# Performance work log

Measured on AMD Instinct MI355X. Metric: run time of the kernel, lower is better.

The kernel has to match this reference:

```python
import jax, jax.numpy as jnp
import numpy as np

H = 4096       # hidden_size
D_IN = 8192    # intermediate_size
N = 16         # ssm_state_size
K = 4          # conv_kernel
R = 256        # time_step_rank
EPS = 1e-6     # mixer_rms_eps


def rms_forward(x, eps=EPS):
    xf = x.astype(jnp.float32)
    var = jnp.mean(xf * xf, axis=-1, keepdims=True)
    return (xf * jax.lax.rsqrt(var + eps)).astype(x.dtype)


def setup_inputs() -> dict:
    key = jax.random.key(0)
    ks = jax.random.split(key, 10)
    s = 0.02
    hidden_states = jax.random.normal(ks[0], (2, 1024, H), dtype=jnp.float32)
    W_in = jax.random.normal(ks[1], (2 * D_IN, H), dtype=jnp.float32) * s
    conv_w = jax.random.normal(ks[2], (D_IN, K), dtype=jnp.float32) * 0.2
    conv_b = jax.random.normal(ks[3], (D_IN,), dtype=jnp.float32) * 0.02
    W_x = jax.random.normal(ks[4], (R + 2 * N, D_IN), dtype=jnp.float32) * s
    W_dt = jax.random.normal(ks[5], (D_IN, R), dtype=jnp.float32) * s
    b_dt = jax.random.normal(ks[6], (D_IN,), dtype=jnp.float32) * 0.02
    A_log = jnp.log(jnp.broadcast_to(jnp.arange(1, N + 1, dtype=jnp.float32)[None, :], (D_IN, N)))
    D = jnp.ones((D_IN,), dtype=jnp.float32)
    W_out = jax.random.normal(ks[7], (H, D_IN), dtype=jnp.float32) * s
    return {"hidden_states": hidden_states, "W_in": W_in, "conv_w": conv_w,
            "conv_b": conv_b, "W_x": W_x, "W_dt": W_dt, "b_dt": b_dt,
            "A_log": A_log, "D": D, "W_out": W_out}


def reference(hidden_states, W_in, conv_w, conv_b, W_x, W_dt, b_dt, A_log, D, W_out):
    b, L, _ = hidden_states.shape
    # in_proj -> split into x and gate  [b, L, d_in] each
    proj = hidden_states @ W_in.T
    x, gate = proj[..., :D_IN], proj[..., D_IN:]
    # depthwise causal conv1d over time (padding K-1, keep first L) + SiLU
    xpad = jnp.pad(x, ((0, 0), (K - 1, 0), (0, 0)))
    xc = conv_b
    for j in range(K):
        xc = xc + conv_w[:, j] * xpad[:, j:j + L, :]
    x = jax.nn.silu(xc)                               # [b, L, d_in]
    # x_proj -> dt / B / C, each RMS-normalized (weightless, FalconMamba)
    ssm = x @ W_x.T                                   # [b, L, R+2N]
    ts, Bm, Cm = ssm[..., :R], ssm[..., R:R + N], ssm[..., R + N:]
    ts = rms_forward(ts)
    Bm = rms_forward(Bm)
    Cm = rms_forward(Cm)
    dt = jax.nn.softplus(ts @ W_dt.T + b_dt)          # [b, L, d_in]
    A = -jnp.exp(A_log.astype(jnp.float32))           # [d_in, N]
    # selective scan over time: state [b, d_in, N]
    def step(state, inp):
        dt_t, B_t, C_t, u_t = inp                     # [b,d],[b,N],[b,N],[b,d]
        dA = jnp.exp(dt_t[..., None] * A)             # [b, d_in, N]
        state = state * dA + (dt_t * u_t)[..., None] * B_t[:, None, :]
        y = jnp.einsum('bdn,bn->bd', state, C_t)
        return state, y
    init = jnp.zeros((b, D_IN, N), dtype=jnp.float32)
    xs = (dt.transpose(1, 0, 2), Bm.transpose(1, 0, 2),
          Cm.transpose(1, 0, 2), x.transpose(1, 0, 2))
    _, ys = jax.lax.scan(step, init, xs)              # [L, b, d_in]
    y = ys.transpose(1, 0, 2) + x * D                 # skip with D
    y = y * jax.nn.silu(gate)                         # gated output
    return y @ W_out.T                                # [b, L, H]
```

## Files before the change

### kernel.cpp

```cpp
#include <hip/hip_runtime.h>
#include <hip/hip_bf16.h>

#define DIN 8192
#define HH 4096
#define BLT 2048
#define LSEQ 1024
#define CL 64
#define NCG 32

typedef unsigned short u16;
typedef __bf16 bf16x8 __attribute__((ext_vector_type(8)));
typedef float f32x4v __attribute__((ext_vector_type(4)));

__device__ __forceinline__ u16 f2b(float f) {
  unsigned u = __float_as_uint(f);
  u += 0x7fff + ((u >> 16) & 1);
  return (u16)(u >> 16);
}
__device__ __forceinline__ float b2f(u16 h) {
  return __uint_as_float(((unsigned)h) << 16);
}

__device__ __forceinline__ void gl_lds16(const u16* g, u16* l) {
  __builtin_amdgcn_global_load_lds(
      (const __attribute__((address_space(1))) void*)g,
      (__attribute__((address_space(3))) void*)l, 16, 0, 0);
}

__device__ __forceinline__ int bsw(int r) { return (r & 3) ^ ((r >> 2) & 3); }

__global__ void cvt_kernel(const float* __restrict__ in, u16* __restrict__ out, long n) {
  long i = ((long)blockIdx.x * blockDim.x + threadIdx.x) * 4;
  long stride = (long)gridDim.x * blockDim.x * 4;
  for (; i < n; i += stride) {
    f32x4v v = *(const f32x4v*)(in + i);
    ushort4 o;
    o.x = f2b(v[0]); o.y = f2b(v[1]); o.z = f2b(v[2]); o.w = f2b(v[3]);
    *(ushort4*)(out + i) = o;
  }
}

__global__ void cvt_pad_kernel(const float* __restrict__ in, u16* __restrict__ out,
                               int rows_in, int cols, long n_out) {
  long i = ((long)blockIdx.x * blockDim.x + threadIdx.x) * 4;
  long stride = (long)gridDim.x * blockDim.x * 4;
  for (; i < n_out; i += stride) {
    long r = i / cols;
    long c = i - r * cols;
    ushort4 o;
    if (r < rows_in) {
      f32x4v v = *(const f32x4v*)(in + r * cols + c);
      o.x = f2b(v[0]); o.y = f2b(v[1]); o.z = f2b(v[2]); o.w = f2b(v[3]);
    } else {
      o.x = 0; o.y = 0; o.z = 0; o.w = 0;
    }
    *(ushort4*)(out + i) = o;
  }
}

__global__ void add2_kernel(const float* __restrict__ a, const float* __restrict__ b,
                            float* __restrict__ o, long n) {
  long i = ((long)blockIdx.x * blockDim.x + threadIdx.x) * 4;
  long stride = (long)gridDim.x * blockDim.x * 4;
  for (; i < n; i += stride) {
    f32x4v va = *(const f32x4v*)(a + i);
    f32x4v vb = *(const f32x4v*)(b + i);
    *(f32x4v*)(o + i) = va + vb;
  }
}

template<int MODE>
__global__ __launch_bounds__(256) void gemm_bt(
    const u16* __restrict__ A, const u16* __restrict__ B, void* __restrict__ Cp,
    int M, int N, int Klen, int lda, const float* __restrict__ bias = nullptr)
{
  __shared__ __align__(16) u16 As[128 * 32];
  __shared__ __align__(16) u16 Bs[128 * 32];
  const int tid = threadIdx.x;
  const int wave = tid >> 6;
  const int lane = tid & 63;
  const int wr = wave >> 1;
  const int wc = wave & 1;
  const long m0 = (long)blockIdx.y * 128;
  const long n0 = (long)blockIdx.x * 128;
  const long kbase = (long)blockIdx.z * Klen;
  const int fr = lane & 15;
  const int fq = lane >> 4;
  const int fs = fq ^ bsw(fr);

  f32x4v acc[4][4];
#pragma unroll
  for (int i = 0; i < 4; ++i)
#pragma unroll
    for (int j = 0; j < 4; ++j) acc[i][j] = (f32x4v){0.f, 0.f, 0.f, 0.f};

  const int srow = tid >> 2;
  const int sseg0 = (tid & 3) ^ bsw(srow);

  for (int k0 = 0; k0 < Klen; k0 += 32) {
#pragma unroll
    for (int i = 0; i < 2; ++i) {
      const int row = srow + i * 64;
      gl_lds16(A + (m0 + row) * (long)lda + kbase + k0 + sseg0 * 8, As + (i * 256 + wave * 64) * 8);
      gl_lds16(B + (n0 + row) * (long)lda + kbase + k0 + sseg0 * 8, Bs + (i * 256 + wave * 64) * 8);
    }
    __syncthreads();
    bf16x8 af[4], bfr[4];
#pragma unroll
    for (int mi = 0; mi < 4; ++mi)
      af[mi] = *(const bf16x8*)(As + (wr * 64 + mi * 16 + fr) * 32 + fs * 8);
#pragma unroll
    for (int ni = 0; ni < 4; ++ni)
      bfr[ni] = *(const bf16x8*)(Bs + (wc * 64 + ni * 16 + fr) * 32 + fs * 8);
#pragma unroll
    for (int mi = 0; mi < 4; ++mi)
#pragma unroll
      for (int ni = 0; ni < 4; ++ni)
        acc[mi][ni] = __builtin_amdgcn_mfma_f32_16x16x32_bf16(af[mi], bfr[ni], acc[mi][ni], 0, 0, 0);
    __syncthreads();
  }

  float* Cf = (float*)Cp + (size_t)blockIdx.z * M * N;
#pragma unroll
  for (int mi = 0; mi < 4; ++mi) {
#pragma unroll
    for (int ni = 0; ni < 4; ++ni) {
      const long col = n0 + wc * 64 + ni * 16 + fr;
#pragma unroll
      for (int r = 0; r < 4; ++r) {
        const long rowi = m0 + wr * 64 + mi * 16 + fq * 4 + r;
        if constexpr (MODE == 0) {
          Cf[rowi * N + col] = acc[mi][ni][r];
        } else {
          const float z = acc[mi][ni][r] + bias[rowi];
          const float dtv = (z > 20.f) ? z : log1pf(__expf(z));
          ((float*)Cp)[rowi * N + col] = dtv;
        }
      }
    }
  }
}

template<int OUTBF>
__global__ __launch_bounds__(512, 2) void gemm256(
    const u16* __restrict__ A, const u16* __restrict__ B, void* __restrict__ Cp,
    int M, int N, int Kfull, int Ksub)
{
  __shared__ __align__(16) u16 lds[3][2][8192];
  const int tid = threadIdx.x;
  const int lane = tid & 63;
  const int wid = tid >> 6;
  const int wm = wid >> 2;
  const int wn = wid & 3;
  const int fr = lane & 15;
  const int fq = lane >> 4;
  const int fs = fq ^ bsw(fr);

  const int nbx = N >> 8;
  const int cpx = gridDim.x >> 3;
  const int bid = blockIdx.x;
  const int swz = (bid & 7) * cpx + (bid >> 3);
  const long m0 = (long)(swz / nbx) << 8;
  const long n0 = (long)(swz % nbx) << 8;
  const long kbase = (long)blockIdx.y * Ksub;

  const int srow = tid >> 2;
  const int sseg = (tid & 3) ^ bsw(srow);
  const u16* ag0 = A + (m0 + srow) * (long)Kfull + kbase + sseg * 8;
  const u16* ag1 = ag0 + 128 * (long)Kfull;
  const u16* bg0 = B + (n0 + srow) * (long)Kfull + kbase + sseg * 8;
  const u16* bg1 = bg0 + 128 * (long)Kfull;

  auto stageA = [&](int c, int koff) {
    gl_lds16(ag0 + koff, &lds[c][0][tid * 8]);
    gl_lds16(bg0 + koff, &lds[c][1][tid * 8]);
  };
  auto stageB = [&](int c, int koff) {
    gl_lds16(ag1 + koff, &lds[c][0][4096 + tid * 8]);
    gl_lds16(bg1 + koff, &lds[c][1][4096 + tid * 8]);
  };

  const int NT = Ksub >> 5;
  stageA(0, 0); stageB(0, 0);
  stageA(1, 32); stageB(1, 32);
  asm volatile("s_waitcnt vmcnt(4)" ::: "memory");
  __builtin_amdgcn_s_barrier();

  f32x4v acc[8][4];
#pragma unroll
  for (int i = 0; i < 8; ++i)
#pragma unroll
    for (int j = 0; j < 4; ++j) acc[i][j] = (f32x4v){0.f, 0.f, 0.f, 0.f};

  const int aoff = (wm * 128 + fr) * 32 + fs * 8;
  const int boff = (wn * 64 + fr) * 32 + fs * 8;
  bf16x8 af[4], bfg[4], al[4];

  int c = 0, cs = 2;
  for (int t = 0; t < NT; ++t) {
    const u16* Asl = &lds[c][0][0];
    const u16* Bsl = &lds[c][1][0];
    const bool pf = (t + 2 < NT);
#pragma unroll
    for (int mi = 0; mi < 4; ++mi) af[mi] = *(const bf16x8*)(Asl + aoff + mi * 512);
#pragma unroll
    for (int ni = 0; ni < 4; ++ni) bfg[ni] = *(const bf16x8*)(Bsl + boff + ni * 512);
    if (pf) stageA(cs, (t + 2) * 32);
    __builtin_amdgcn_s_barrier();
    asm volatile("s_waitcnt lgkmcnt(0)" ::: "memory");
    __builtin_amdgcn_sched_barrier(0);
    __builtin_amdgcn_s_setprio(1);
#pragma unroll
    for (int mi = 0; mi < 4; ++mi)
#pragma unroll
      for (int ni = 0; ni < 4; ++ni)
        acc[mi][ni] = __builtin_amdgcn_mfma_f32_16x16x32_bf16(af[mi], bfg[ni], acc[mi][ni], 0, 0, 0);
    __builtin_amdgcn_s_setprio(0);
#pragma unroll
    for (int mi = 0; mi < 4; ++mi) al[mi] = *(const bf16x8*)(Asl + aoff + 2048 + mi * 512);
    if (pf) stageB(cs, (t + 2) * 32);
    __builtin_amdgcn_s_barrier();
    asm volatile("s_waitcnt lgkmcnt(0)" ::: "memory");
    __builtin_amdgcn_sched_barrier(0);
    __builtin_amdgcn_s_setprio(1);
#pragma unroll
    for (int mi = 0; mi < 4; ++mi)
#pragma unroll
      for (int ni = 0; ni < 4; ++ni)
        acc[mi + 4][ni] = __builtin_amdgcn_mfma_f32_16x16x32_bf16(al[mi], bfg[ni], acc[mi + 4][ni], 0, 0, 0);
    __builtin_amdgcn_s_setprio(0);
    if (pf) {
      asm volatile("s_waitcnt vmcnt(4)" ::: "memory");
    } else {
      asm volatile("s_waitcnt vmcnt(0)" ::: "memory");
    }
    __builtin_amdgcn_s_barrier();
    c = (c == 2) ? 0 : c + 1;
    cs = (cs == 2) ? 0 : cs + 1;
  }

  float* Cf = (float*)Cp + (size_t)blockIdx.y * M * N;
#pragma unroll
  for (int mi = 0; mi < 8; ++mi) {
#pragma unroll
    for (int ni = 0; ni < 4; ++ni) {
      const long col = n0 + wn * 64 + ni * 16 + fr;
      const long rbase = m0 + wm * 128 + mi * 16 + fq * 4;
#pragma unroll
      for (int r = 0; r < 4; ++r) {
        if constexpr (OUTBF) {
          ((u16*)Cp)[(rbase + r) * N + col] = f2b(acc[mi][ni][r]);
        } else {
          Cf[(rbase + r) * N + col] = acc[mi][ni][r];
        }
      }
    }
  }
}

__global__ __launch_bounds__(256) void conv_silu_kernel(
    const u16* __restrict__ proj, const float* __restrict__ conv_w,
    const float* __restrict__ conv_b, u16* __restrict__ xb)
{
  const int idx = blockIdx.x * 256 + threadIdx.x;
  const int tok = idx >> 11;
  const int dq = (idx & 2047) << 2;
  const int l = tok & (LSEQ - 1);
  f32x4v cb = *(const f32x4v*)(conv_b + dq);
  float a0 = cb[0], a1 = cb[1], a2 = cb[2], a3 = cb[3];
  f32x4v w0 = *(const f32x4v*)(conv_w + (size_t)(dq + 0) * 4);
  f32x4v w1 = *(const f32x4v*)(conv_w + (size_t)(dq + 1) * 4);
  f32x4v w2 = *(const f32x4v*)(conv_w + (size_t)(dq + 2) * 4);
  f32x4v w3 = *(const f32x4v*)(conv_w + (size_t)(dq + 3) * 4);
#pragma unroll
  for (int j = 0; j < 4; ++j) {
    const int lj = l - 3 + j;
    if (lj >= 0) {
      ushort4 xv = *(const ushort4*)(proj + (size_t)(tok - 3 + j) * 16384 + dq);
      a0 = fmaf(w0[j], b2f(xv.x), a0);
      a1 = fmaf(w1[j], b2f(xv.y), a1);
      a2 = fmaf(w2[j], b2f(xv.z), a2);
      a3 = fmaf(w3[j], b2f(xv.w), a3);
    }
  }
  ushort4 o;
  o.x = f2b(a0 / (1.f + __expf(-a0)));
  o.y = f2b(a1 / (1.f + __expf(-a1)));
  o.z = f2b(a2 / (1.f + __expf(-a2)));
  o.w = f2b(a3 / (1.f + __expf(-a3)));
  *(ushort4*)(xb + (size_t)tok * DIN + dq) = o;
}

__global__ __launch_bounds__(256) void transpose_x_kernel(
    const u16* __restrict__ in, u16* __restrict__ outp)
{
  const int t = threadIdx.x;
  const int sr = t >> 4, sc = t & 15;
  const long r0 = (long)blockIdx.x * 64 + sr * 4;
  const long c0 = (long)blockIdx.y * 64 + sc * 4;
  ushort4 v[4];
#pragma unroll
  for (int i = 0; i < 4; ++i)
    v[i] = *(const ushort4*)(in + (r0 + i) * DIN + c0);
#pragma unroll
  for (int i = 0; i < 4; ++i) {
    ushort4 o;
    o.x = ((const u16*)&v[0])[i];
    o.y = ((const u16*)&v[1])[i];
    o.z = ((const u16*)&v[2])[i];
    o.w = ((const u16*)&v[3])[i];
    *(ushort4*)(outp + (c0 + i) * BLT + r0) = o;
  }
}

__global__ __launch_bounds__(64) void rms_kernel(
    const float* __restrict__ part, u16* __restrict__ tsb,
    float* __restrict__ Bn, float* __restrict__ Cn)
{
  const int tok = blockIdx.x;
  const int lane = threadIdx.x;
  const size_t rowoff = (size_t)tok * 384;
  f32x4v t = (f32x4v){0.f, 0.f, 0.f, 0.f};
#pragma unroll
  for (int s = 0; s < 8; ++s)
    t += *(const f32x4v*)(part + (size_t)s * (BLT * 384) + rowoff + lane * 4);
  float ss = t[0]*t[0] + t[1]*t[1] + t[2]*t[2] + t[3]*t[3];
#pragma unroll
  for (int o = 32; o; o >>= 1) ss += __shfl_xor(ss, o);
  const float sc = rsqrtf(ss * (1.f / 256.f) + 1e-6f);
  ushort4 o4;
  o4.x = f2b(t[0] * sc); o4.y = f2b(t[1] * sc);
  o4.z = f2b(t[2] * sc); o4.w = f2b(t[3] * sc);
  *(ushort4*)(tsb + (size_t)tok * 256 + lane * 4) = o4;

  float v = 0.f;
  if (lane < 32) {
#pragma unroll
    for (int s = 0; s < 8; ++s)
      v += part[(size_t)s * (BLT * 384) + rowoff + 256 + lane];
  }
  float g = v * v;
#pragma unroll
  for (int o = 1; o < 16; o <<= 1) g += __shfl_xor(g, o);
  const float scBC = rsqrtf(g * (1.f / 16.f) + 1e-6f);
  if (lane < 16) Bn[(size_t)tok * 16 + lane] = v * scBC;
  else if (lane < 32) Cn[(size_t)tok * 16 + (lane - 16)] = v * scBC;
}

__global__ __launch_bounds__(256) void scan_p1_kernel(
    const float* __restrict__ dtT, const u16* __restrict__ xT,
    const float* __restrict__ Bn, const float* __restrict__ A_log,
    float* __restrict__ partE, float* __restrict__ partS)
{
  __shared__ float Bsh[CL][16];
  const int tid = threadIdx.x;
  const int chunk = blockIdx.y;
  const int d = blockIdx.x * 64 + (tid >> 2);
  const int ln = tid & 3;
  const int tok0 = chunk * CL;
  {
    const int tt = tid >> 2, q = tid & 3;
    *(f32x4v*)&Bsh[tt][q * 4] = *(const f32x4v*)(Bn + (size_t)(tok0 + tt) * 16 + q * 4);
  }
  __syncthreads();
  float a[4];
#pragma unroll
  for (int j = 0; j < 4; ++j) a[j] = -__expf(A_log[(size_t)d * 16 + ln * 4 + j]);
  float E0 = 1.f, E1 = 1.f, E2 = 1.f, E3 = 1.f;
  float S0 = 0.f, S1 = 0.f, S2 = 0.f, S3 = 0.f;
  const float* dtp = dtT + (size_t)d * BLT + tok0;
  const u16* xp = xT + (size_t)d * BLT + tok0;
  for (int l = 0; l < CL; l += 4) {
    f32x4v dt4 = *(const f32x4v*)(dtp + l);
    ushort4 u4 = *(const ushort4*)(xp + l);
#pragma unroll
    for (int i = 0; i < 4; ++i) {
      const float dt = dt4[i];
      const float u = b2f(((const u16*)&u4)[i]);
      const float dtu = dt * u;
      f32x4v Bv = *(const f32x4v*)&Bsh[l + i][ln * 4];
      const float e0 = __expf(dt * a[0]);
      const float e1 = __expf(dt * a[1]);
      const float e2 = __expf(dt * a[2]);
      const float e3 = __expf(dt * a[3]);
      S0 = fmaf(S0, e0, dtu * Bv[0]); E0 *= e0;
      S1 = fmaf(S1, e1, dtu * Bv[1]); E1 *= e1;
      S2 = fmaf(S2, e2, dtu * Bv[2]); E2 *= e2;
      S3 = fmaf(S3, e3, dtu * Bv[3]); E3 *= e3;
    }
  }
  const size_t off = (size_t)chunk * (DIN * 16) + (size_t)d * 16 + ln * 4;
  f32x4v Ev = {E0, E1, E2, E3}, Sv = {S0, S1, S2, S3};
  *(f32x4v*)(partE + off) = Ev;
  *(f32x4v*)(partS + off) = Sv;
}

__global__ __launch_bounds__(256) void scan_p2_kernel(
    const float* __restrict__ partE, float* __restrict__ partS)
{
  const int dn = blockIdx.x * 256 + threadIdx.x;
  float s = 0.f;
  for (int c = 0; c < NCG; ++c) {
    if ((c & 15) == 0) s = 0.f;
    const size_t off = (size_t)c * (DIN * 16) + dn;
    const float e = partE[off];
    const float ps = partS[off];
    partS[off] = s;
    s = fmaf(e, s, ps);
  }
}

__global__ __launch_bounds__(256) void scan_p3_kernel(
    const float* __restrict__ dtT, const u16* __restrict__ xT,
    const float* __restrict__ Bn, const float* __restrict__ Cn,
    const float* __restrict__ A_log, const float* __restrict__ Dv,
    const float* __restrict__ stateIn, const u16* __restrict__ proj,
    u16* __restrict__ yg)
{
  __shared__ float Bsh[CL][16], Csh[CL][16];
  const int tid = threadIdx.x;
  const int chunk = blockIdx.y;
  const int d = blockIdx.x * 64 + (tid >> 2);
  const int ln = tid & 3;
  const int tok0 = chunk * CL;
  {
    const int tt = tid >> 2, q = tid & 3;
    *(f32x4v*)&Bsh[tt][q * 4] = *(const f32x4v*)(Bn + (size_t)(tok0 + tt) * 16 + q * 4);
    *(f32x4v*)&Csh[tt][q * 4] = *(const f32x4v*)(Cn + (size_t)(tok0 + tt) * 16 + q * 4);
  }
  __syncthreads();
  float a[4];
#pragma unroll
  for (int j = 0; j < 4; ++j) a[j] = -__expf(A_log[(size_t)d * 16 + ln * 4 + j]);
  f32x4v sv = *(const f32x4v*)(stateIn + (size_t)chunk * (DIN * 16) + (size_t)d * 16 + ln * 4);
  float S0 = sv[0], S1 = sv[1], S2 = sv[2], S3 = sv[3];
  const float Dd = Dv[d];
  const float* dtp = dtT + (size_t)d * BLT + tok0;
  const u16* xp = xT + (size_t)d * BLT + tok0;
  for (int l = 0; l < CL; l += 4) {
    f32x4v dt4 = *(const f32x4v*)(dtp + l);
    ushort4 u4 = *(const ushort4*)(xp + l);
#pragma unroll
    for (int i = 0; i < 4; ++i) {
      const float dt = dt4[i];
      const float u = b2f(((const u16*)&u4)[i]);
      const float dtu = dt * u;
      f32x4v Bv = *(const f32x4v*)&Bsh[l + i][ln * 4];
      f32x4v Cv = *(const f32x4v*)&Csh[l + i][ln * 4];
      const float e0 = __expf(dt * a[0]);
      const float e1 = __expf(dt * a[1]);
      const float e2 = __expf(dt * a[2]);
      const float e3 = __expf(dt * a[3]);
      float y;
      S0 = fmaf(S0, e0, dtu * Bv[0]); y = S0 * Cv[0];
      S1 = fmaf(S1, e1, dtu * Bv[1]); y = fmaf(S1, Cv[1], y);
      S2 = fmaf(S2, e2, dtu * Bv[2]); y = fmaf(S2, Cv[2], y);
      S3 = fmaf(S3, e3, dtu * Bv[3]); y = fmaf(S3, Cv[3], y);
      y += __shfl_xor(y, 1);
      y += __shfl_xor(y, 2);
      if (ln == 0) {
        const long tok = tok0 + l + i;
        const float yt = fmaf(u, Dd, y);
        const float gt = b2f(proj[tok * 16384 + DIN + d]);
        const float sg = gt / (1.f + __expf(-gt));
        yg[tok * DIN + d] = f2b(yt * sg);
      }
    }
  }
}

extern "C" void kernel_launch(void* const* d_in, const int* in_sizes, int n_in,
                              void* d_out, int out_size, void* d_ws, size_t ws_size,
                              hipStream_t stream) {
  const float* hs     = (const float*)d_in[0];
  const float* W_in   = (const float*)d_in[1];
  const float* conv_w = (const float*)d_in[2];
  const float* conv_b = (const float*)d_in[3];
  const float* W_x    = (const float*)d_in[4];
  const float* W_dt   = (const float*)d_in[5];
  const float* b_dt   = (const float*)d_in[6];
  const float* A_log  = (const float*)d_in[7];
  const float* Dv     = (const float*)d_in[8];
  const float* W_out  = (const float*)d_in[9];
  float* out = (float*)d_out;

  char* ws = (char*)d_ws;
  size_t off = 0;
  auto alloc = [&](size_t bytes) -> char* {
    char* p = ws + off;
    off += (bytes + 255) & ~(size_t)255;
    return p;
  };

  u16* W_in_b = (u16*)alloc(134217728);
  u16* hs_b = (u16*)alloc(16777216);
  u16* proj_b = (u16*)alloc((size_t)BLT * 16384 * 2);
  u16* x_b    = (u16*)alloc((size_t)BLT * DIN * 2);
  u16* W_xp_b = (u16*)alloc((size_t)384 * DIN * 2);
  u16* yg_b   = (u16*)alloc((size_t)BLT * DIN * 2);
  u16* x_T    = (u16*)alloc((size_t)BLT * DIN * 2);

  float* dt_T    = (float*)W_in_b;
  u16*   W_out_b = (u16*)((char*)W_in_b + 67108864);
  u16*   ts_b    = (u16*)((char*)hs_b + 3145728);
  float* Bn      = (float*)((char*)hs_b + 3145728 + 1048576);
  float* Cn      = (float*)((char*)hs_b + 3145728 + 1048576 + 131072);
  u16*   W_dt_b  = (u16*)((char*)hs_b + 3145728 + 1048576 + 262144);
  float* partE   = (float*)x_b;
  float* partS   = (float*)((char*)x_b + 16777216);
  float* ssm_part= (float*)yg_b;
  float* out_part= (float*)proj_b;

  const int CG = 2048;
  cvt_kernel<<<CG, 256, 0, stream>>>(W_in, W_in_b, 67108864L);
  cvt_kernel<<<CG, 256, 0, stream>>>(hs, hs_b, 8388608L);
  gemm256<1><<<dim3((16384 / 256) * (BLT / 256), 1), 512, 0, stream>>>(hs_b, W_in_b, proj_b, BLT, 16384, 4096, 4096);
  cvt_kernel<<<CG, 256, 0, stream>>>(W_out, W_out_b, 33554432L);
  cvt_kernel<<<CG, 256, 0, stream>>>(W_dt, W_dt_b, 2097152L);
  cvt_pad_kernel<<<CG, 256, 0, stream>>>(W_x, W_xp_b, 288, DIN, (long)384 * DIN);
  conv_silu_kernel<<<16384, 256, 0, stream>>>(proj_b, conv_w, conv_b, x_b);
  transpose_x_kernel<<<dim3(BLT / 64, DIN / 64), 256, 0, stream>>>(x_b, x_T);
  gemm_bt<0><<<dim3(384 / 128, BLT / 128, 8), 256, 0, stream>>>(x_b, W_xp_b, ssm_part, BLT, 384, 1024, DIN, nullptr);
  rms_kernel<<<BLT, 64, 0, stream>>>(ssm_part, ts_b, Bn, Cn);
  gemm_bt<3><<<dim3(BLT / 128, DIN / 128), 256, 0, stream>>>(W_dt_b, ts_b, dt_T, DIN, BLT, 256, 256, b_dt);
  scan_p1_kernel<<<dim3(DIN / 64, NCG), 256, 0, stream>>>(dt_T, x_T, Bn, A_log, partE, partS);
  scan_p2_kernel<<<DIN * 16 / 256, 256, 0, stream>>>(partE, partS);
  scan_p3_kernel<<<dim3(DIN / 64, NCG), 256, 0, stream>>>(dt_T, x_T, Bn, Cn, A_log, Dv, partS, proj_b, yg_b);
  gemm256<0><<<dim3((HH / 256) * (BLT / 256), 2), 512, 0, stream>>>(yg_b, W_out_b, out_part, BLT, HH, DIN, DIN / 2);
  add2_kernel<<<CG, 256, 0, stream>>>(out_part, out_part + (size_t)BLT * HH, out, (long)BLT * HH);
}
```

Measured before the change: 944.2 us.

## Fuse conv+SiLU with x transpose and stage gate/output through LDS in scan

Merges the depthwise conv+SiLU kernel with the separate transpose kernel, so each block computes a 64x64 tile, writes the row-major copy and also transposes through shared memory to write x_T. This removes one kernel launch and the re-read of x from global memory. In scan_p3, the gate values are prefetched coalesced into LDS and outputs are buffered in LDS, then written as coalesced rows instead of strided per-element global accesses. The cost is extra shared memory and syncs, and some LDS bank conflicts from the column-wise reads.

```diff
diff --git a/kernel.cpp b/kernel.cpp
--- a/kernel.cpp
+++ b/kernel.cpp
@@ -258,59 +258,57 @@
   }
 }
 
-__global__ __launch_bounds__(256) void conv_silu_kernel(
+__global__ __launch_bounds__(256) void conv_silu_tr_kernel(
     const u16* __restrict__ proj, const float* __restrict__ conv_w,
-    const float* __restrict__ conv_b, u16* __restrict__ xb)
-{
-  const int idx = blockIdx.x * 256 + threadIdx.x;
-  const int tok = idx >> 11;
-  const int dq = (idx & 2047) << 2;
-  const int l = tok & (LSEQ - 1);
-  f32x4v cb = *(const f32x4v*)(conv_b + dq);
-  float a0 = cb[0], a1 = cb[1], a2 = cb[2], a3 = cb[3];
-  f32x4v w0 = *(const f32x4v*)(conv_w + (size_t)(dq + 0) * 4);
-  f32x4v w1 = *(const f32x4v*)(conv_w + (size_t)(dq + 1) * 4);
-  f32x4v w2 = *(const f32x4v*)(conv_w + (size_t)(dq + 2) * 4);
-  f32x4v w3 = *(const f32x4v*)(conv_w + (size_t)(dq + 3) * 4);
-#pragma unroll
-  for (int j = 0; j < 4; ++j) {
-    const int lj = l - 3 + j;
-    if (lj >= 0) {
-      ushort4 xv = *(const ushort4*)(proj + (size_t)(tok - 3 + j) * 16384 + dq);
-      a0 = fmaf(w0[j], b2f(xv.x), a0);
-      a1 = fmaf(w1[j], b2f(xv.y), a1);
-      a2 = fmaf(w2[j], b2f(xv.z), a2);
-      a3 = fmaf(w3[j], b2f(xv.w), a3);
-    }
-  }
-  ushort4 o;
-  o.x = f2b(a0 / (1.f + __expf(-a0)));
-  o.y = f2b(a1 / (1.f + __expf(-a1)));
-  o.z = f2b(a2 / (1.f + __expf(-a2)));
-  o.w = f2b(a3 / (1.f + __expf(-a3)));
-  *(ushort4*)(xb + (size_t)tok * DIN + dq) = o;
-}
-
-__global__ __launch_bounds__(256) void transpose_x_kernel(
-    const u16* __restrict__ in, u16* __restrict__ outp)
-{
+    const float* __restrict__ conv_b, u16* __restrict__ xb, u16* __restrict__ xT)
+{
+  __shared__ u16 xt[64][68];
   const int t = threadIdx.x;
-  const int sr = t >> 4, sc = t & 15;
-  const long r0 = (long)blockIdx.x * 64 + sr * 4;
-  const long c0 = (long)blockIdx.y * 64 + sc * 4;
-  ushort4 v[4];
-#pragma unroll
-  for (int i = 0; i < 4; ++i)
-    v[i] = *(const ushort4*)(in + (r0 + i) * DIN + c0);
-#pragma unroll
-  for (int i = 0; i < 4; ++i) {
+  const int tr = t >> 4;
+  const int dqi = t & 15;
+  const long tok0 = (long)blockIdx.x * 64;
+  const int d0 = blockIdx.y * 64;
+  const int d = d0 + dqi * 4;
+  f32x4v cb = *(const f32x4v*)(conv_b + d);
+  f32x4v w0 = *(const f32x4v*)(conv_w + (size_t)(d + 0) * 4);
+  f32x4v w1 = *(const f32x4v*)(conv_w + (size_t)(d + 1) * 4);
+  f32x4v w2 = *(const f32x4v*)(conv_w + (size_t)(d + 2) * 4);
+  f32x4v w3 = *(const f32x4v*)(conv_w + (size_t)(d + 3) * 4);
+#pragma unroll
+  for (int tt = 0; tt < 4; ++tt) {
+    const long tok = tok0 + tr + tt * 16;
+    const int l = (int)(tok & (LSEQ - 1));
+    float a0 = cb[0], a1 = cb[1], a2 = cb[2], a3 = cb[3];
+#pragma unroll
+    for (int j = 0; j < 4; ++j) {
+      const int lj = l - 3 + j;
+      if (lj >= 0) {
+        ushort4 xv = *(const ushort4*)(proj + (tok - 3 + j) * 16384 + d);
+        a0 = fmaf(w0[j], b2f(xv.x), a0);
+        a1 = fmaf(w1[j], b2f(xv.y), a1);
+        a2 = fmaf(w2[j], b2f(xv.z), a2);
+        a3 = fmaf(w3[j], b2f(xv.w), a3);
+      }
+    }
     ushort4 o;
-    o.x = ((const u16*)&v[0])[i];
-    o.y = ((const u16*)&v[1])[i];
-    o.z = ((const u16*)&v[2])[i];
-    o.w = ((const u16*)&v[3])[i];
-    *(ushort4*)(outp + (c0 + i) * BLT + r0) = o;
-  }
+    o.x = f2b(a0 / (1.f + __expf(-a0)));
+    o.y = f2b(a1 / (1.f + __expf(-a1)));
+    o.z = f2b(a2 / (1.f + __expf(-a2)));
+    o.w = f2b(a3 / (1.f + __expf(-a3)));
+    *(ushort4*)(xb + tok * DIN + d) = o;
+    *(ushort4*)(&xt[tr + tt * 16][dqi * 4]) = o;
+  }
+  __syncthreads();
+  const int dl = t >> 2;
+  const int tq = t & 3;
+  u16 buf[16];
+#pragma unroll
+  for (int i = 0; i < 16; ++i) buf[i] = xt[tq * 16 + i][dl];
+  u16* dst = xT + (size_t)(d0 + dl) * BLT + tok0 + tq * 16;
+  *(ushort4*)(dst + 0)  = *(ushort4*)&buf[0];
+  *(ushort4*)(dst + 4)  = *(ushort4*)&buf[4];
+  *(ushort4*)(dst + 8)  = *(ushort4*)&buf[8];
+  *(ushort4*)(dst + 12) = *(ushort4*)&buf[12];
 }
 
 __global__ __launch_bounds__(64) void rms_kernel(
@@ -418,15 +416,22 @@
     u16* __restrict__ yg)
 {
   __shared__ float Bsh[CL][16], Csh[CL][16];
+  __shared__ u16 gsh[CL][64], ysh[CL][64];
   const int tid = threadIdx.x;
   const int chunk = blockIdx.y;
-  const int d = blockIdx.x * 64 + (tid >> 2);
+  const int d0 = blockIdx.x * 64;
+  const int dch = tid >> 2;
+  const int d = d0 + dch;
   const int ln = tid & 3;
   const int tok0 = chunk * CL;
   {
     const int tt = tid >> 2, q = tid & 3;
     *(f32x4v*)&Bsh[tt][q * 4] = *(const f32x4v*)(Bn + (size_t)(tok0 + tt) * 16 + q * 4);
     *(f32x4v*)&Csh[tt][q * 4] = *(const f32x4v*)(Cn + (size_t)(tok0 + tt) * 16 + q * 4);
+    const u16* grow = proj + (size_t)(tok0 + tt) * 16384 + DIN + d0 + q * 16;
+#pragma unroll
+    for (int qq = 0; qq < 4; ++qq)
+      *(ushort4*)&gsh[tt][q * 16 + qq * 4] = *(const ushort4*)(grow + qq * 4);
   }
   __syncthreads();
   float a[4];
@@ -459,13 +464,20 @@
       y += __shfl_xor(y, 1);
       y += __shfl_xor(y, 2);
       if (ln == 0) {
-        const long tok = tok0 + l + i;
         const float yt = fmaf(u, Dd, y);
-        const float gt = b2f(proj[tok * 16384 + DIN + d]);
+        const float gt = b2f(gsh[l + i][dch]);
         const float sg = gt / (1.f + __expf(-gt));
-        yg[tok * DIN + d] = f2b(yt * sg);
+        ysh[l + i][dch] = f2b(yt * sg);
       }
     }
+  }
+  __syncthreads();
+  {
+    const int tt = tid >> 2, q = tid & 3;
+    u16* yrow = yg + (size_t)(tok0 + tt) * DIN + d0 + q * 16;
+#pragma unroll
+    for (int qq = 0; qq < 4; ++qq)
+      *(ushort4*)(yrow + qq * 4) = *(ushort4*)&ysh[tt][q * 16 + qq * 4];
   }
 }
 
@@ -518,8 +530,7 @@
   cvt_kernel<<<CG, 256, 0, stream>>>(W_out, W_out_b, 33554432L);
   cvt_kernel<<<CG, 256, 0, stream>>>(W_dt, W_dt_b, 2097152L);
   cvt_pad_kernel<<<CG, 256, 0, stream>>>(W_x, W_xp_b, 288, DIN, (long)384 * DIN);
-  conv_silu_kernel<<<16384, 256, 0, stream>>>(proj_b, conv_w, conv_b, x_b);
-  transpose_x_kernel<<<dim3(BLT / 64, DIN / 64), 256, 0, stream>>>(x_b, x_T);
+  conv_silu_tr_kernel<<<dim3(BLT / 64, DIN / 64), 256, 0, stream>>>(proj_b, conv_w, conv_b, x_b, x_T);
   gemm_bt<0><<<dim3(384 / 128, BLT / 128, 8), 256, 0, stream>>>(x_b, W_xp_b, ssm_part, BLT, 384, 1024, DIN, nullptr);
   rms_kernel<<<BLT, 64, 0, stream>>>(ssm_part, ts_b, Bn, Cn);
   gemm_bt<3><<<dim3(BLT / 128, DIN / 128), 256, 0, stream>>>(W_dt_b, ts_b, dt_T, DIN, BLT, 256, 256, b_dt);
```

Measured after the change: 908.0 us. 1.04x faster.
